# Kernel tuning notes

Hardware: AMD Instinct MI355X
Metric: run time of the kernel (lower is better)

The kernel has to match this reference:

```python
import jax, jax.numpy as jnp
import numpy as np

EMBED = 4096
HEADS = 16
HEAD_DIM = EMBED // HEADS  # 256
ROT = 64                   # rotary_dim
B, S = 1, 2048
MASK_VAL = -1.0e9          # masked_bias


def setup_inputs() -> dict:
    key = jax.random.key(0)
    ks = jax.random.split(key, 5)
    sc = 0.02
    return {
        "hidden_states": jax.random.normal(ks[0], (B, S, EMBED), jnp.float32),
        "Wq": jax.random.normal(ks[1], (EMBED, EMBED), jnp.float32) * sc,
        "Wk": jax.random.normal(ks[2], (EMBED, EMBED), jnp.float32) * sc,
        "Wv": jax.random.normal(ks[3], (EMBED, EMBED), jnp.float32) * sc,
        "Wo": jax.random.normal(ks[4], (EMBED, EMBED), jnp.float32) * sc,
    }


def _rotate_every_two(x):
    # interleave: (x0,x1,x2,x3,...) -> (x1,x0,x3,x2,...)  [as written in source]
    r = jnp.stack((x[..., 1::2], x[..., ::2]), axis=-1)
    return r.reshape(x.shape)


def _fixed_pos_embedding(seq_len, rot_dim):
    inv_freq = 1.0 / (10000.0 ** (jnp.arange(0, rot_dim, 2, dtype=jnp.float32) / rot_dim))
    t = jnp.arange(seq_len, dtype=jnp.float32)
    sinusoid = jnp.einsum('i,j->ij', t, inv_freq)  # [S, rot_dim/2]
    return jnp.sin(sinusoid), jnp.cos(sinusoid)


def _apply_rotary(x, sin, cos):
    # x: [B, S, H, ROT]; sin/cos: [S, ROT/2] -> repeat each freq twice along last dim
    sin = jnp.repeat(sin[None, :, None, :], 2, axis=3)
    cos = jnp.repeat(cos[None, :, None, :], 2, axis=3)
    return x * cos + _rotate_every_two(x) * sin


def reference(hidden_states, Wq, Wk, Wv, Wo):
    b, s, e = hidden_states.shape
    q = (hidden_states @ Wq).reshape(b, s, HEADS, HEAD_DIM)
    k = (hidden_states @ Wk).reshape(b, s, HEADS, HEAD_DIM)
    v = (hidden_states @ Wv).reshape(b, s, HEADS, HEAD_DIM)

    sin, cos = _fixed_pos_embedding(s, ROT)
    q = jnp.concatenate([_apply_rotary(q[..., :ROT], sin, cos), q[..., ROT:]], axis=-1)
    k = jnp.concatenate([_apply_rotary(k[..., :ROT], sin, cos), k[..., ROT:]], axis=-1)

    q = q.transpose(0, 2, 1, 3)  # [B,H,S,D]
    k = k.transpose(0, 2, 1, 3)
    v = v.transpose(0, 2, 1, 3)

    logits = jnp.einsum('bhqd,bhkd->bhqk', q, k)  # [B,H,S,S]
    causal = jnp.tril(jnp.ones((s, s), dtype=bool))[None, None]
    # GPT-J quirk: mask applied BEFORE scaling
    logits = jnp.where(causal, logits, MASK_VAL)
    logits = logits / jnp.sqrt(jnp.float32(HEAD_DIM))
    attn = jax.nn.softmax(logits, axis=-1)

    out = jnp.einsum('bhqk,bhkd->bhqd', attn, v)
    out = out.transpose(0, 2, 1, 3).reshape(b, s, e)
    return out @ Wo
```

## Files before the change

### kernel.cpp

```cpp
#include <hip/hip_runtime.h>
#include <hip/hip_bf16.h>
#include <math.h>

#define EMBED 4096
#define SLEN 2048
#define HEADS 16
#define HDIM 256
#define ROT 64

typedef __bf16 bf16;
typedef __attribute__((ext_vector_type(8))) __bf16 bf16x8;
typedef __attribute__((ext_vector_type(4))) float f32x4;

__device__ __forceinline__ void async_copy16(const void* g, void* l) {
  __builtin_amdgcn_global_load_lds((const __attribute__((address_space(1))) void*)g,
                                   (__attribute__((address_space(3))) void*)l,
                                   16, 0, 0);
}

__global__ __launch_bounds__(256) void cast_kernel(const float* __restrict__ in,
                                                   bf16* __restrict__ out, int n4) {
  int i = blockIdx.x * 256 + threadIdx.x;
  if (i >= n4) return;
  float4 v = ((const float4*)in)[i];
  bf16 o[4] __attribute__((aligned(8)));
  o[0] = (bf16)v.x; o[1] = (bf16)v.y; o[2] = (bf16)v.z; o[3] = (bf16)v.w;
  ((ushort4*)out)[i] = *(const ushort4*)o;
}

__global__ __launch_bounds__(256) void transpose_cast(const float* __restrict__ W,
                                                      bf16* __restrict__ Wt) {
  __shared__ bf16 tile[64][65];
  int k0 = blockIdx.y * 64, n0 = blockIdx.x * 64;
  int tr = threadIdx.x >> 4, tc = threadIdx.x & 15;
#pragma unroll
  for (int i = 0; i < 4; i++) {
    int row = tr + i * 16;
    float4 v = *(const float4*)(W + (size_t)(k0 + row) * EMBED + n0 + tc * 4);
    tile[row][tc * 4 + 0] = (bf16)v.x;
    tile[row][tc * 4 + 1] = (bf16)v.y;
    tile[row][tc * 4 + 2] = (bf16)v.z;
    tile[row][tc * 4 + 3] = (bf16)v.w;
  }
  __syncthreads();
#pragma unroll
  for (int i = 0; i < 4; i++) {
    int nl = tr + i * 16;
    bf16 o[4] __attribute__((aligned(8)));
#pragma unroll
    for (int j = 0; j < 4; j++) o[j] = tile[tc * 4 + j][nl];
    *(ushort4*)(Wt + (size_t)(n0 + nl) * EMBED + k0 + tc * 4) = *(const ushort4*)o;
  }
}

template <int MODE>
__global__ __launch_bounds__(512, 1) void gemm_pipe(const bf16* __restrict__ A,
                                                    const bf16* __restrict__ Bt,
                                                    void* __restrict__ Cout,
                                                    int M, int N, int K) {
  constexpr int BM = 128, BN = 256, BK = 64;
  __shared__ __align__(16) bf16 As[3][BM * BK];
  __shared__ __align__(16) bf16 Bs[3][BN * BK];
  int t = threadIdx.x;
  int lane = t & 63, w = t >> 6;
  int c16 = lane & 15, g4 = lane >> 4;
  int wm = w >> 2, wn = w & 3;
  int m0 = blockIdx.y * BM, n0 = blockIdx.x * BN;
  int nt = K / BK;

  f32x4 acc[4][4] = {};

  auto stageA1 = [&](const bf16* Asrc, bf16* Ad, int i) {
    int c = i * 512 + t;
    int row = c >> 3, col8 = c & 7;
    async_copy16(Asrc + (size_t)row * K + ((col8 ^ (row & 7)) * 8), Ad + c * 8);
  };
  auto stageB1 = [&](const bf16* Bsrc, bf16* Bd, int i) {
    int c = i * 512 + t;
    int row = c >> 3, col8 = c & 7;
    async_copy16(Bsrc + (size_t)row * K + ((col8 ^ (row & 7)) * 8), Bd + c * 8);
  };

#pragma unroll
  for (int kt0 = 0; kt0 < 2; kt0++) {
    const bf16* Asrc = A + (size_t)m0 * K + kt0 * BK;
    const bf16* Bsrc = Bt + (size_t)n0 * K + kt0 * BK;
#pragma unroll
    for (int i = 0; i < 2; i++) stageA1(Asrc, As[kt0], i);
#pragma unroll
    for (int i = 0; i < 4; i++) stageB1(Bsrc, Bs[kt0], i);
  }
  asm volatile("s_waitcnt vmcnt(6)" ::: "memory");
  __builtin_amdgcn_s_barrier();

  for (int kt = 0; kt < nt; kt++) {
    int slot = kt - (kt / 3) * 3;
    int s2 = (kt + 2) - ((kt + 2) / 3) * 3;
    const bf16* Ab = As[slot];
    const bf16* Bb = Bs[slot];
    bool do_stage = (kt + 2 < nt);
    const bf16* Asrc = A + (size_t)m0 * K + (kt + 2) * BK;
    const bf16* Bsrc = Bt + (size_t)n0 * K + (kt + 2) * BK;
    bf16* Ad = As[s2];
    bf16* Bd = Bs[s2];

    {
      bf16x8 af[4], bfr[4];
#pragma unroll
      for (int fm = 0; fm < 4; fm++) {
        int row = wm * 64 + fm * 16 + c16;
        af[fm] = *(const bf16x8*)(Ab + row * BK + ((g4 ^ (row & 7)) * 8));
      }
#pragma unroll
      for (int fn = 0; fn < 4; fn++) {
        int row = wn * 64 + fn * 16 + c16;
        bfr[fn] = *(const bf16x8*)(Bb + row * BK + ((g4 ^ (row & 7)) * 8));
      }
      if (do_stage) {
        stageA1(Asrc, Ad, 0);
        stageA1(Asrc, Ad, 1);
        stageB1(Bsrc, Bd, 0);
        stageB1(Bsrc, Bd, 1);
      }
      __builtin_amdgcn_s_barrier();
      asm volatile("s_waitcnt lgkmcnt(0)" ::: "memory");
      __builtin_amdgcn_sched_barrier(0);
      __builtin_amdgcn_s_setprio(1);
#pragma unroll
      for (int fm = 0; fm < 4; fm++)
#pragma unroll
        for (int fn = 0; fn < 4; fn++)
          acc[fm][fn] = __builtin_amdgcn_mfma_f32_16x16x32_bf16(af[fm], bfr[fn],
                                                                acc[fm][fn], 0, 0, 0);
      __builtin_amdgcn_s_setprio(0);
      __builtin_amdgcn_s_barrier();
    }
    {
      bf16x8 af[4], bfr[4];
#pragma unroll
      for (int fm = 0; fm < 4; fm++) {
        int row = wm * 64 + fm * 16 + c16;
        af[fm] = *(const bf16x8*)(Ab + row * BK + (((4 + g4) ^ (row & 7)) * 8));
      }
#pragma unroll
      for (int fn = 0; fn < 4; fn++) {
        int row = wn * 64 + fn * 16 + c16;
        bfr[fn] = *(const bf16x8*)(Bb + row * BK + (((4 + g4) ^ (row & 7)) * 8));
      }
      if (do_stage) {
        stageB1(Bsrc, Bd, 2);
        stageB1(Bsrc, Bd, 3);
      }
      __builtin_amdgcn_s_barrier();
      asm volatile("s_waitcnt lgkmcnt(0)" ::: "memory");
      __builtin_amdgcn_sched_barrier(0);
      __builtin_amdgcn_s_setprio(1);
#pragma unroll
      for (int fm = 0; fm < 4; fm++)
#pragma unroll
        for (int fn = 0; fn < 4; fn++)
          acc[fm][fn] = __builtin_amdgcn_mfma_f32_16x16x32_bf16(af[fm], bfr[fn],
                                                                acc[fm][fn], 0, 0, 0);
      __builtin_amdgcn_s_setprio(0);
      if (kt < nt - 2) {
        asm volatile("s_waitcnt vmcnt(6)" ::: "memory");
      } else if (kt == nt - 2) {
        asm volatile("s_waitcnt vmcnt(0)" ::: "memory");
      }
      __builtin_amdgcn_s_barrier();
    }
  }

#pragma unroll
  for (int fm = 0; fm < 4; fm++) {
#pragma unroll
    for (int fn = 0; fn < 4; fn++) {
      int col = n0 + wn * 64 + fn * 16 + c16;
#pragma unroll
      for (int r = 0; r < 4; r++) {
        int row = m0 + wm * 64 + fm * 16 + g4 * 4 + r;
        float v = acc[fm][fn][r];
        if (MODE == 1) {
          int d = col & (HDIM - 1);
          if (d < ROT) {
            float pv = __shfl_xor(v, 1);
            int jj = d >> 1;
            float invf = __expf(-0.28782313662425575f * (float)jj);
            float ang = (float)row * invf;
            float sa, ca;
            sincosf(ang, &sa, &ca);
            v = v * ca + pv * sa;
          }
        }
        if (MODE == 3) {
          ((float*)Cout)[(size_t)row * N + col] = v;
        } else if (MODE == 2) {
          ((bf16*)Cout)[(size_t)col * M + row] = (bf16)v;
        } else {
          ((bf16*)Cout)[(size_t)row * N + col] = (bf16)v;
        }
      }
    }
  }
}

__global__ __launch_bounds__(256, 1) void attn_kernel(const bf16* __restrict__ Q,
                                                      const bf16* __restrict__ Kmat,
                                                      const bf16* __restrict__ Vt,
                                                      bf16* __restrict__ O) {
  __shared__ __align__(16) bf16 Ks[2][64 * 256];
  __shared__ __align__(16) bf16 Vs[2][64 * 256];
  __shared__ __align__(16) bf16 Pl[4][16 * 64];
  int t = threadIdx.x, lane = t & 63, w = t >> 6;
  int c16 = lane & 15, g4 = lane >> 4;
  int b = blockIdx.x;
  int h = (b & 7) * 2 + ((b >> 3) & 1);
  int pair = b >> 4;

  for (int pass = 0; pass < 2; ++pass) {
    int qt = pass ? (31 - pair) : pair;
    int q0w = qt * 64 + w * 16;

    bf16x8 qf[8];
    {
      const bf16* qp = Q + (size_t)(q0w + c16) * EMBED + h * HDIM + g4 * 8;
#pragma unroll
      for (int kk = 0; kk < 8; kk++) qf[kk] = *(const bf16x8*)(qp + kk * 32);
    }
    f32x4 acco[16] = {};
    float mrow[4], lrow[4];
#pragma unroll
    for (int r = 0; r < 4; r++) { mrow[r] = -1e30f; lrow[r] = 0.f; }

    __syncthreads();
#pragma unroll
    for (int j = 0; j < 8; j++) {
      int c = j * 256 + w * 64 + lane;
      int row = c >> 5, col8 = c & 31;
      int scol = (col8 ^ (row & 7)) * 8;
      async_copy16(Kmat + (size_t)(0 * 64 + row) * EMBED + h * HDIM + scol,
                   Ks[0] + (size_t)c * 8);
    }
#pragma unroll
    for (int j = 0; j < 8; j++) {
      int c = j * 256 + w * 64 + lane;
      int row = c >> 3, col8 = c & 7;
      int scol = (col8 ^ (row & 7)) * 8;
      async_copy16(Vt + (size_t)(h * HDIM + row) * SLEN + 0 * 64 + scol,
                   Vs[0] + (size_t)c * 8);
    }
    __syncthreads();

    for (int kt = 0; kt <= qt; kt++) {
      int cur = kt & 1;
      if (kt < qt) {
#pragma unroll
        for (int j = 0; j < 8; j++) {
          int c = j * 256 + w * 64 + lane;
          int row = c >> 5, col8 = c & 31;
          int scol = (col8 ^ (row & 7)) * 8;
          async_copy16(Kmat + (size_t)((kt + 1) * 64 + row) * EMBED + h * HDIM + scol,
                       Ks[cur ^ 1] + (size_t)c * 8);
        }
#pragma unroll
        for (int j = 0; j < 8; j++) {
          int c = j * 256 + w * 64 + lane;
          int row = c >> 3, col8 = c & 7;
          int scol = (col8 ^ (row & 7)) * 8;
          async_copy16(Vt + (size_t)(h * HDIM + row) * SLEN + (kt + 1) * 64 + scol,
                       Vs[cur ^ 1] + (size_t)c * 8);
        }
      }
      const bf16* KsB = Ks[cur];
      const bf16* VsB = Vs[cur];

      f32x4 accs[4] = {};
      __builtin_amdgcn_s_setprio(1);
#pragma unroll
      for (int kk = 0; kk < 8; kk++) {
#pragma unroll
        for (int fn = 0; fn < 4; fn++) {
          int r = fn * 16 + c16;
          bf16x8 kf = *(const bf16x8*)(KsB + r * 256 + ((kk * 4 + g4) ^ (c16 & 7)) * 8);
          accs[fn] = __builtin_amdgcn_mfma_f32_16x16x32_bf16(qf[kk], kf, accs[fn], 0, 0, 0);
        }
      }
      __builtin_amdgcn_s_setprio(0);

      float pm[4][4];
      bool diag = (kt == qt);
#pragma unroll
      for (int fn = 0; fn < 4; fn++)
#pragma unroll
        for (int r = 0; r < 4; r++) {
          float s = accs[fn][r] * 0.0625f;
          if (diag) {
            int kg = fn * 16 + c16;
            int qg = w * 16 + g4 * 4 + r;
            if (kg > qg) s = -1e30f;
          }
          pm[fn][r] = s;
        }
      float tmx[4];
#pragma unroll
      for (int r = 0; r < 4; r++) {
        float mx = fmaxf(fmaxf(pm[0][r], pm[1][r]), fmaxf(pm[2][r], pm[3][r]));
#pragma unroll
        for (int off = 1; off < 16; off <<= 1) mx = fmaxf(mx, __shfl_xor(mx, off));
        tmx[r] = mx;
      }
      bool need = false;
#pragma unroll
      for (int r = 0; r < 4; r++) need = need || (tmx[r] > mrow[r] + 8.0f);
      if (__any(need)) {
#pragma unroll
        for (int r = 0; r < 4; r++) {
          float mn = fmaxf(mrow[r], tmx[r]);
          float sc = __expf(mrow[r] - mn);
          mrow[r] = mn;
          lrow[r] *= sc;
#pragma unroll
          for (int fd = 0; fd < 16; fd++) acco[fd][r] *= sc;
        }
      }
      float rs[4] = {0.f, 0.f, 0.f, 0.f};
#pragma unroll
      for (int fn = 0; fn < 4; fn++)
#pragma unroll
        for (int r = 0; r < 4; r++) {
          float p = __expf(pm[fn][r] - mrow[r]);
          pm[fn][r] = p;
          rs[r] += p;
        }
#pragma unroll
      for (int r = 0; r < 4; r++) {
#pragma unroll
        for (int off = 1; off < 16; off <<= 1) rs[r] += __shfl_xor(rs[r], off);
        lrow[r] += rs[r];
      }
#pragma unroll
      for (int fn = 0; fn < 4; fn++)
#pragma unroll
        for (int r = 0; r < 4; r++) {
          int q = g4 * 4 + r;
          int chunk = (fn * 2 + (c16 >> 3)) ^ (q & 7);
          Pl[w][q * 64 + chunk * 8 + (c16 & 7)] = (bf16)pm[fn][r];
        }
      __builtin_amdgcn_s_setprio(1);
#pragma unroll
      for (int kk2 = 0; kk2 < 2; kk2++) {
        bf16x8 pf = *(const bf16x8*)(&Pl[w][c16 * 64 + ((kk2 * 4 + g4) ^ (c16 & 7)) * 8]);
#pragma unroll
        for (int fd = 0; fd < 16; fd++) {
          int rv = fd * 16 + c16;
          bf16x8 vf = *(const bf16x8*)(VsB + rv * 64 + ((kk2 * 4 + g4) ^ (c16 & 7)) * 8);
          acco[fd] = __builtin_amdgcn_mfma_f32_16x16x32_bf16(pf, vf, acco[fd], 0, 0, 0);
        }
      }
      __builtin_amdgcn_s_setprio(0);
      __syncthreads();
    }
    float inv[4];
#pragma unroll
    for (int r = 0; r < 4; r++) inv[r] = 1.0f / lrow[r];
#pragma unroll
    for (int fd = 0; fd < 16; fd++)
#pragma unroll
      for (int r = 0; r < 4; r++) {
        int qg = q0w + g4 * 4 + r;
        int col = h * HDIM + fd * 16 + c16;
        O[(size_t)qg * EMBED + col] = (bf16)(acco[fd][r] * inv[r]);
      }
  }
}

extern "C" void kernel_launch(void* const* d_in, const int* in_sizes, int n_in,
                              void* d_out, int out_size, void* d_ws, size_t ws_size,
                              hipStream_t stream) {
  const float* hidden = (const float*)d_in[0];
  const float* Wq = (const float*)d_in[1];
  const float* Wk = (const float*)d_in[2];
  const float* Wv = (const float*)d_in[3];
  const float* Wo = (const float*)d_in[4];
  float* out = (float*)d_out;

  char* ws = (char*)d_ws;
  const size_t SZ_H = (size_t)SLEN * EMBED * 2;
  const size_t SZ_W = (size_t)EMBED * EMBED * 2;
  if (ws_size < 5 * SZ_H + SZ_W) return;

  bf16* h_bf = (bf16*)ws;
  bf16* Wt   = (bf16*)(ws + SZ_H);
  bf16* Qb   = (bf16*)(ws + SZ_H + SZ_W);
  bf16* Kb   = (bf16*)(ws + 2 * SZ_H + SZ_W);
  bf16* Vtb  = (bf16*)(ws + 3 * SZ_H + SZ_W);
  bf16* Ob   = (bf16*)(ws + 4 * SZ_H + SZ_W);

  cast_kernel<<<(SLEN * EMBED / 4 + 255) / 256, 256, 0, stream>>>(hidden, h_bf,
                                                                  SLEN * EMBED / 4);

  dim3 tgrid(EMBED / 64, EMBED / 64);
  dim3 ggrid(EMBED / 256, SLEN / 128);

  transpose_cast<<<tgrid, 256, 0, stream>>>(Wq, Wt);
  gemm_pipe<1><<<ggrid, 512, 0, stream>>>(h_bf, Wt, Qb, SLEN, EMBED, EMBED);

  transpose_cast<<<tgrid, 256, 0, stream>>>(Wk, Wt);
  gemm_pipe<1><<<ggrid, 512, 0, stream>>>(h_bf, Wt, Kb, SLEN, EMBED, EMBED);

  transpose_cast<<<tgrid, 256, 0, stream>>>(Wv, Wt);
  gemm_pipe<2><<<ggrid, 512, 0, stream>>>(h_bf, Wt, Vtb, SLEN, EMBED, EMBED);

  attn_kernel<<<dim3(256), 256, 0, stream>>>(Qb, Kb, Vtb, Ob);

  transpose_cast<<<tgrid, 256, 0, stream>>>(Wo, Wt);
  gemm_pipe<3><<<ggrid, 512, 0, stream>>>(Ob, Wt, out, SLEN, EMBED, EMBED);
}
```

Baseline: 523.7 us.

## Use 128-row query tiles with 8 waves sharing each K/V tile in attention

The attention kernel moves from 256 threads handling two 64-row query tiles, in balanced pairs, to 512 threads (8 waves) handling one 128-row query tile per block, ordered longest-first. Each K/V tile loaded into LDS now serves twice as many query rows, halving K/V global traffic per query. Causal masking now uses global indices, and waves whose rows lie before a tile skip its compute. The trade-off: the paired-tile load balancing is lost and some waves idle on the last diagonal tile.

```diff
diff --git a/kernel.cpp b/kernel.cpp
--- a/kernel.cpp
+++ b/kernel.cpp
@@ -204,73 +204,70 @@
   }
 }
 
-__global__ __launch_bounds__(256, 1) void attn_kernel(const bf16* __restrict__ Q,
+__global__ __launch_bounds__(512, 1) void attn_kernel(const bf16* __restrict__ Q,
                                                       const bf16* __restrict__ Kmat,
                                                       const bf16* __restrict__ Vt,
                                                       bf16* __restrict__ O) {
   __shared__ __align__(16) bf16 Ks[2][64 * 256];
   __shared__ __align__(16) bf16 Vs[2][64 * 256];
-  __shared__ __align__(16) bf16 Pl[4][16 * 64];
+  __shared__ __align__(16) bf16 Pl[8][16 * 64];
   int t = threadIdx.x, lane = t & 63, w = t >> 6;
   int c16 = lane & 15, g4 = lane >> 4;
   int b = blockIdx.x;
-  int h = (b & 7) * 2 + ((b >> 3) & 1);
-  int pair = b >> 4;
-
-  for (int pass = 0; pass < 2; ++pass) {
-    int qt = pass ? (31 - pair) : pair;
-    int q0w = qt * 64 + w * 16;
-
-    bf16x8 qf[8];
-    {
-      const bf16* qp = Q + (size_t)(q0w + c16) * EMBED + h * HDIM + g4 * 8;
-#pragma unroll
-      for (int kk = 0; kk < 8; kk++) qf[kk] = *(const bf16x8*)(qp + kk * 32);
-    }
-    f32x4 acco[16] = {};
-    float mrow[4], lrow[4];
-#pragma unroll
-    for (int r = 0; r < 4; r++) { mrow[r] = -1e30f; lrow[r] = 0.f; }
-
-    __syncthreads();
-#pragma unroll
-    for (int j = 0; j < 8; j++) {
-      int c = j * 256 + w * 64 + lane;
-      int row = c >> 5, col8 = c & 31;
-      int scol = (col8 ^ (row & 7)) * 8;
-      async_copy16(Kmat + (size_t)(0 * 64 + row) * EMBED + h * HDIM + scol,
-                   Ks[0] + (size_t)c * 8);
-    }
-#pragma unroll
-    for (int j = 0; j < 8; j++) {
-      int c = j * 256 + w * 64 + lane;
-      int row = c >> 3, col8 = c & 7;
-      int scol = (col8 ^ (row & 7)) * 8;
-      async_copy16(Vt + (size_t)(h * HDIM + row) * SLEN + 0 * 64 + scol,
-                   Vs[0] + (size_t)c * 8);
-    }
-    __syncthreads();
-
-    for (int kt = 0; kt <= qt; kt++) {
-      int cur = kt & 1;
-      if (kt < qt) {
-#pragma unroll
-        for (int j = 0; j < 8; j++) {
-          int c = j * 256 + w * 64 + lane;
-          int row = c >> 5, col8 = c & 31;
-          int scol = (col8 ^ (row & 7)) * 8;
-          async_copy16(Kmat + (size_t)((kt + 1) * 64 + row) * EMBED + h * HDIM + scol,
-                       Ks[cur ^ 1] + (size_t)c * 8);
-        }
-#pragma unroll
-        for (int j = 0; j < 8; j++) {
-          int c = j * 256 + w * 64 + lane;
-          int row = c >> 3, col8 = c & 7;
-          int scol = (col8 ^ (row & 7)) * 8;
-          async_copy16(Vt + (size_t)(h * HDIM + row) * SLEN + (kt + 1) * 64 + scol,
-                       Vs[cur ^ 1] + (size_t)c * 8);
-        }
-      }
+  int h = b & 15;
+  int qt = 15 - (b >> 4);
+  int q0w = qt * 128 + w * 16;
+  int ktmax = 2 * qt + 1;
+
+  bf16x8 qf[8];
+  {
+    const bf16* qp = Q + (size_t)(q0w + c16) * EMBED + h * HDIM + g4 * 8;
+#pragma unroll
+    for (int kk = 0; kk < 8; kk++) qf[kk] = *(const bf16x8*)(qp + kk * 32);
+  }
+  f32x4 acco[16] = {};
+  float mrow[4], lrow[4];
+#pragma unroll
+  for (int r = 0; r < 4; r++) { mrow[r] = -1e30f; lrow[r] = 0.f; }
+
+#pragma unroll
+  for (int j = 0; j < 4; j++) {
+    int c = j * 512 + t;
+    int row = c >> 5, col8 = c & 31;
+    async_copy16(Kmat + (size_t)row * EMBED + h * HDIM + ((col8 ^ (row & 7)) * 8),
+                 Ks[0] + (size_t)c * 8);
+  }
+#pragma unroll
+  for (int j = 0; j < 4; j++) {
+    int c = j * 512 + t;
+    int row = c >> 3, col8 = c & 7;
+    async_copy16(Vt + (size_t)(h * HDIM + row) * SLEN + ((col8 ^ (row & 7)) * 8),
+                 Vs[0] + (size_t)c * 8);
+  }
+  __syncthreads();
+
+  for (int kt = 0; kt <= ktmax; kt++) {
+    int cur = kt & 1;
+    if (kt < ktmax) {
+#pragma unroll
+      for (int j = 0; j < 4; j++) {
+        int c = j * 512 + t;
+        int row = c >> 5, col8 = c & 31;
+        async_copy16(Kmat + (size_t)((kt + 1) * 64 + row) * EMBED + h * HDIM +
+                         ((col8 ^ (row & 7)) * 8),
+                     Ks[cur ^ 1] + (size_t)c * 8);
+      }
+#pragma unroll
+      for (int j = 0; j < 4; j++) {
+        int c = j * 512 + t;
+        int row = c >> 3, col8 = c & 7;
+        async_copy16(Vt + (size_t)(h * HDIM + row) * SLEN + (kt + 1) * 64 +
+                         ((col8 ^ (row & 7)) * 8),
+                     Vs[cur ^ 1] + (size_t)c * 8);
+      }
+    }
+    bool active = (kt * 64 <= q0w + 15);
+    if (active) {
       const bf16* KsB = Ks[cur];
       const bf16* VsB = Vs[cur];
 
@@ -288,15 +285,15 @@
       __builtin_amdgcn_s_setprio(0);
 
       float pm[4][4];
-      bool diag = (kt == qt);
+      bool diag = (kt * 64 + 63 > q0w);
 #pragma unroll
       for (int fn = 0; fn < 4; fn++)
 #pragma unroll
         for (int r = 0; r < 4; r++) {
           float s = accs[fn][r] * 0.0625f;
           if (diag) {
-            int kg = fn * 16 + c16;
-            int qg = w * 16 + g4 * 4 + r;
+            int kg = kt * 64 + fn * 16 + c16;
+            int qg = q0w + g4 * 4 + r;
             if (kg > qg) s = -1e30f;
           }
           pm[fn][r] = s;
@@ -358,20 +355,20 @@
         }
       }
       __builtin_amdgcn_s_setprio(0);
-      __syncthreads();
-    }
-    float inv[4];
-#pragma unroll
-    for (int r = 0; r < 4; r++) inv[r] = 1.0f / lrow[r];
-#pragma unroll
-    for (int fd = 0; fd < 16; fd++)
-#pragma unroll
-      for (int r = 0; r < 4; r++) {
-        int qg = q0w + g4 * 4 + r;
-        int col = h * HDIM + fd * 16 + c16;
-        O[(size_t)qg * EMBED + col] = (bf16)(acco[fd][r] * inv[r]);
-      }
-  }
+    }
+    __syncthreads();
+  }
+  float inv[4];
+#pragma unroll
+  for (int r = 0; r < 4; r++) inv[r] = 1.0f / lrow[r];
+#pragma unroll
+  for (int fd = 0; fd < 16; fd++)
+#pragma unroll
+    for (int r = 0; r < 4; r++) {
+      int qg = q0w + g4 * 4 + r;
+      int col = h * HDIM + fd * 16 + c16;
+      O[(size_t)qg * EMBED + col] = (bf16)(acco[fd][r] * inv[r]);
+    }
 }
 
 extern "C" void kernel_launch(void* const* d_in, const int* in_sizes, int n_in,
@@ -411,7 +408,7 @@
   transpose_cast<<<tgrid, 256, 0, stream>>>(Wv, Wt);
   gemm_pipe<2><<<ggrid, 512, 0, stream>>>(h_bf, Wt, Vtb, SLEN, EMBED, EMBED);
 
-  attn_kernel<<<dim3(256), 256, 0, stream>>>(Qb, Kb, Vtb, Ob);
+  attn_kernel<<<dim3(256), 512, 0, stream>>>(Qb, Kb, Vtb, Ob);
 
   transpose_cast<<<tgrid, 256, 0, stream>>>(Wo, Wt);
   gemm_pipe<3><<<ggrid, 512, 0, stream>>>(Ob, Wt, out, SLEN, EMBED, EMBED);
```

Result: slower. 539.3 us (+3.0%).
